# Optimization experiments

Hardware: AMD Instinct MI355X
Metric: run time of the kernel (lower is better)

The kernel has to match this reference:

```python
import jax, jax.numpy as jnp
import numpy as np

E = 1024
H = 16
HD = 64
LN_EPS = 1e-5


def _layernorm(x, g, b):
    mu = jnp.mean(x, axis=-1, keepdims=True)
    var = jnp.mean((x - mu) ** 2, axis=-1, keepdims=True)
    return (x - mu) * jax.lax.rsqrt(var + LN_EPS) * g + b


def _positional(L):
    # PositionalEncoding: stepper = 1/10000^(arange(0,E,2)/E); cat(sin, cos) -> [L, E]
    stepper = 1.0 / (10000.0 ** (jnp.arange(0, E, 2, dtype=jnp.float32) / E))
    args = jnp.arange(L, dtype=jnp.float32)[:, None] * stepper[None, :]  # [L, E/2]
    return jnp.concatenate([jnp.sin(args), jnp.cos(args)], axis=1)  # [L, E]


def setup_inputs() -> dict:
    key = jax.random.key(0)
    ks = jax.random.split(key, 8)
    s = 1.0 / np.sqrt(E)
    return {
        "sequences": jax.random.normal(ks[0], (4, 2048, E), dtype=jnp.float32),
        "W_q": jax.random.normal(ks[1], (E, E), dtype=jnp.float32) * s,
        "W_k": jax.random.normal(ks[2], (E, E), dtype=jnp.float32) * s,
        "W_v": jax.random.normal(ks[3], (E, E), dtype=jnp.float32) * s,
        "W_o": jax.random.normal(ks[4], (E, E), dtype=jnp.float32) * s,
        "ln1_g": jnp.ones((E,), jnp.float32),
        "ln1_b": jnp.zeros((E,), jnp.float32),
        "lin_W": jax.random.normal(ks[5], (E, E), dtype=jnp.float32) * s,  # torch Linear weight [out,in]
        "lin_b": jnp.zeros((E,), jnp.float32),
        "ln2_g": jnp.ones((E,), jnp.float32),
        "ln2_b": jnp.zeros((E,), jnp.float32),
    }


def reference(sequences, W_q, W_k, W_v, W_o, ln1_g, ln1_b, lin_W, lin_b, ln2_g, ln2_b):
    B, L, _ = sequences.shape
    x = sequences + _positional(L)[None]  # add positional embeddings
    # projections (no bias)
    q = (x @ W_q).reshape(B, L, H, HD).transpose(0, 2, 1, 3)  # [B,H,L,hd]
    k = (x @ W_k).reshape(B, L, H, HD).transpose(0, 2, 1, 3)
    v = (x @ W_v).reshape(B, L, H, HD).transpose(0, 2, 1, 3)
    # linear (softmax-free) attention: (Q K^T / sqrt(hd)) V
    scores = jnp.einsum("bhqd,bhkd->bhqk", q, k) / jnp.sqrt(jnp.float32(HD))
    ctx = jnp.einsum("bhqk,bhkd->bhqd", scores, v)
    ctx = ctx.transpose(0, 2, 1, 3).reshape(B, L, E)
    attn_out = ctx @ W_o
    h = _layernorm(x + attn_out, ln1_g, ln1_b)
    ff = jax.nn.relu(h @ lin_W.T + lin_b)
    return _layernorm(ff + h, ln2_g, ln2_b)
```

## Files before the change

kernel.cpp:

```cpp
#include <hip/hip_runtime.h>
#include <cstdint>

typedef unsigned short u16;
typedef __bf16 bf16x8 __attribute__((ext_vector_type(8)));
typedef float f32x4 __attribute__((ext_vector_type(4)));

__device__ __forceinline__ u16 f2bf(float f) {
    unsigned u = __float_as_uint(f);
    u += 0x7fffu + ((u >> 16) & 1u);
    return (u16)(u >> 16);
}
__device__ __forceinline__ float bf2f(u16 h) {
    return __uint_as_float(((unsigned)h) << 16);
}

__device__ __forceinline__ void lds16(const void* g, void* l) {
    __builtin_amdgcn_global_load_lds(
        (const __attribute__((address_space(1))) void*)g,
        (__attribute__((address_space(3))) void*)l, 16, 0, 0);
}

__device__ __forceinline__ float pos_term(int l, int e) {
    const float c = -13.287712379549449f / 512.0f;
    int ii = e & 511;
    float st  = exp2f(c * (float)ii);
    float arg = (float)l * st;
    return (e < 512) ? sinf(arg) : cosf(arg);
}

__global__ __launch_bounds__(256) void prep_all(const float* __restrict__ seq,
                                                const float* __restrict__ wq,
                                                const float* __restrict__ wk,
                                                const float* __restrict__ wv,
                                                const float* __restrict__ wl,
                                                u16* __restrict__ xb,
                                                u16* __restrict__ xt,
                                                u16* __restrict__ wt) {
    const int bx = blockIdx.x;
    const int t = threadIdx.x;
    if (bx < 4096) {
        __shared__ u16 tb[64][33];
        const int rt = bx >> 5, ct = bx & 31;
        const int r0 = rt * 64, c0 = ct * 32;
        const int r_l = t >> 2, c8 = (t & 3) * 8;
        const int row = r0 + r_l, l = row & 2047;
        const float* sp = seq + (size_t)row * 1024 + c0 + c8;
        float4 a0 = ((const float4*)sp)[0];
        float4 a1 = ((const float4*)sp)[1];
        float v[8] = {a0.x, a0.y, a0.z, a0.w, a1.x, a1.y, a1.z, a1.w};
        u16 ob[8];
#pragma unroll
        for (int jj = 0; jj < 8; jj++) {
            v[jj] += pos_term(l, c0 + c8 + jj);
            ob[jj] = f2bf(v[jj]);
            tb[r_l][c8 + jj] = ob[jj];
        }
        u16* xp = xb + (size_t)row * 1024 + c0 + c8;
        ((ushort4*)xp)[0] = *(const ushort4*)&ob[0];
        ((ushort4*)xp)[1] = *(const ushort4*)&ob[4];
        __syncthreads();
        const int c_l = t >> 3, r8 = (t & 7) * 8;
        u16 tv[8];
#pragma unroll
        for (int jj = 0; jj < 8; jj++) tv[jj] = tb[r8 + jj][c_l];
        u16* tp = xt + (size_t)(c0 + c_l) * 8192 + r0 + r8;
        ((ushort4*)tp)[0] = *(const ushort4*)&tv[0];
        ((ushort4*)tp)[1] = *(const ushort4*)&tv[4];
        return;
    }
    const int idx = bx - 4096;
    const int mat = idx >> 10, bxw = idx & 1023;
    const int gx = bxw & 31, gy = bxw >> 5;
    const int tx = t & 31, ty = t >> 5;
    const float* src = (mat == 0) ? wq : (mat == 1) ? wk : (mat == 2) ? wv : wl;
    u16* dst = wt + (size_t)mat * 1024 * 1024;
    if (mat == 0 || mat == 3) {
        int col = gx * 32 + tx, row0 = gy * 32;
#pragma unroll
        for (int j = 0; j < 32; j += 8)
            dst[(size_t)(row0 + ty + j) * 1024 + col] = f2bf(src[(size_t)(row0 + ty + j) * 1024 + col]);
    } else {
        __shared__ float tile[32][33];
        int col = gx * 32 + tx, row0 = gy * 32;
#pragma unroll
        for (int j = 0; j < 32; j += 8)
            tile[ty + j][tx] = src[(size_t)(row0 + ty + j) * 1024 + col];
        __syncthreads();
        int col2 = gy * 32 + tx, row20 = gx * 32;
#pragma unroll
        for (int j = 0; j < 32; j += 8)
            dst[(size_t)(row20 + ty + j) * 1024 + col2] = f2bf(tile[tx][ty + j]);
    }
}

__global__ __launch_bounds__(256) void gram_kernel(const u16* __restrict__ xt,
                                                   u16* __restrict__ G) {
    __shared__ __align__(16) u16 lds[32768];
    const int t = threadIdx.x;
    const int nwg = gridDim.x;
    int bid = (int)blockIdx.x;
    bid = (bid & 7) * (nwg >> 3) + (bid >> 3);
    const int bt = bid >> 6, tile6 = bid & 63;
    const int tm = tile6 >> 3, tn = tile6 & 7;
    const size_t m0 = (size_t)tm << 7, n0 = (size_t)tn << 7;
    const int w = t >> 6, lane = t & 63;
    const int wr = w >> 1, wc = w & 1;
    const size_t lda = 8192;
    const u16* A = xt + (size_t)bt * 2048;

    const int r0 = t >> 3;
    const int ksrc = (t & 7) ^ (r0 & 7);
    const u16* sA = A + (m0 + r0) * lda + ksrc * 8;
    const u16* sB = A + (n0 + r0) * lda + ksrc * 8;
    const size_t st = (size_t)32 * lda;

    const int kx = lane & 7;
    const int ks0 = (((lane >> 4) ^ kx) << 3);
    const int ks1 = (((4 + (lane >> 4)) ^ kx) << 3);
    const int ao = ((wr << 6) | (lane & 15)) << 6;
    const int bo = 8192 + ((((wc << 6) | (lane & 15))) << 6);

    f32x4 acc[4][4];
#pragma unroll
    for (int i = 0; i < 4; i++)
#pragma unroll
        for (int j = 0; j < 4; j++)
#pragma unroll
            for (int r = 0; r < 4; r++) acc[i][j][r] = 0.0f;

#define STAGEG(bb, ko)                                                        \
    do {                                                                      \
        u16* dA_ = lds + (bb) * 16384 + (w << 9);                             \
        u16* dB_ = dA_ + 8192;                                                \
        _Pragma("unroll")                                                     \
        for (int j_ = 0; j_ < 4; j_++) {                                      \
            lds16(sA + (ko) + j_ * st, dA_ + j_ * 2048);                      \
            lds16(sB + (ko) + j_ * st, dB_ + j_ * 2048);                      \
        }                                                                     \
    } while (0)

    const int NT = 32;
    STAGEG(0, 0);
    for (int kt = 0; kt < NT; kt++) {
        const int b = kt & 1;
        asm volatile("" ::: "memory");
        if (kt + 1 < NT) {
            STAGEG(b ^ 1, (size_t)(kt + 1) << 6);
            asm volatile("s_waitcnt vmcnt(8)" ::: "memory");
        } else {
            asm volatile("s_waitcnt vmcnt(0)" ::: "memory");
        }
        __builtin_amdgcn_s_barrier();
        asm volatile("" ::: "memory");
        const u16* Lb = lds + b * 16384;
#pragma unroll
        for (int kc = 0; kc < 2; kc++) {
            const int ksl = kc ? ks1 : ks0;
            bf16x8 af[4], bfr[4];
#pragma unroll
            for (int i = 0; i < 4; i++)
                af[i] = *reinterpret_cast<const bf16x8*>(Lb + ao + i * 1024 + ksl);
#pragma unroll
            for (int j = 0; j < 4; j++)
                bfr[j] = *reinterpret_cast<const bf16x8*>(Lb + bo + j * 1024 + ksl);
            __builtin_amdgcn_s_setprio(1);
#pragma unroll
            for (int i = 0; i < 4; i++)
#pragma unroll
                for (int j = 0; j < 4; j++)
                    acc[i][j] = __builtin_amdgcn_mfma_f32_16x16x32_bf16(af[i], bfr[j], acc[i][j], 0, 0, 0);
            __builtin_amdgcn_s_setprio(0);
        }
        asm volatile("" ::: "memory");
        __builtin_amdgcn_s_barrier();
    }
#undef STAGEG

    u16* C = G + ((size_t)bt << 20);
    const int crow = (lane >> 4) << 2, ccol = lane & 15;
#pragma unroll
    for (int i = 0; i < 4; i++)
#pragma unroll
        for (int j = 0; j < 4; j++) {
            size_t row = m0 + (wr << 6) + (i << 4) + crow;
            size_t col = n0 + (wc << 6) + (j << 4) + ccol;
#pragma unroll
            for (int r = 0; r < 4; r++)
                C[(row + r) * 1024 + col] = f2bf(acc[i][j][r]);
        }
}

template <int EPI>
__global__ __launch_bounds__(512) void gemm8p(const u16* __restrict__ A,
                                              const u16* __restrict__ Bt,
                                              void* __restrict__ Cv,
                                              const float* __restrict__ bias,
                                              int N, int K, int lda, size_t bstride) {
    __shared__ __align__(16) u16 lds[49152];
    const int t = threadIdx.x;
    const int ntn = N >> 8;
    const int nwg = gridDim.x;
    int bid = (int)blockIdx.x;
    bid = (bid & 7) * (nwg >> 3) + (bid >> 3);
    const int tm = bid / ntn, tn = bid - tm * ntn;
    const size_t m0 = (size_t)tm << 7, n0 = (size_t)tn << 8;
    const int w = t >> 6, lane = t & 63;
    const int wr = w >> 2, wc = w & 3;
    const u16* Bt_e = Bt + (bstride ? (m0 >> 11) * bstride : 0);

    const int r0 = t >> 3;
    const int ksrc = (t & 7) ^ (r0 & 7);
    const u16* sA0 = A + (m0 + r0) * (size_t)lda + ksrc * 8;
    const u16* sA1 = sA0 + (size_t)64 * lda;
    const u16* sB0 = Bt_e + (n0 + r0) * (size_t)K + ksrc * 8;
    const u16* sB1 = sB0 + (size_t)64 * K;
    const u16* sB2 = sB0 + (size_t)128 * K;
    const u16* sB3 = sB0 + (size_t)192 * K;
    u16* dstW = lds + (w << 9);

    const int ao = ((wr << 6) | (lane & 15)) << 6;
    const int bo = 8192 + ((((wc << 6) | (lane & 15))) << 6);
    const int kx = lane & 7;
    const int ks0 = (((lane >> 4) ^ kx) << 3);
    const int ks1 = (((4 + (lane >> 4)) ^ kx) << 3);

    f32x4 acc[4][4];
#pragma unroll
    for (int i = 0; i < 4; i++)
#pragma unroll
        for (int j = 0; j < 4; j++)
#pragma unroll
            for (int r = 0; r < 4; r++) acc[i][j][r] = 0.0f;

    const int NT = K >> 6;
    lds16(sA0, dstW);          lds16(sA1, dstW + 4096);
    lds16(sB0, dstW + 8192);   lds16(sB1, dstW + 12288);
    lds16(sB2, dstW + 16384);  lds16(sB3, dstW + 20480);

    for (int kt = 0; kt < NT; kt++) {
        const int b = kt & 1;
        asm volatile("" ::: "memory");
        if (kt + 1 < NT) {
            const size_t ko = (size_t)(kt + 1) << 6;
            u16* d = dstW + (b ^ 1) * 24576;
            lds16(sA0 + ko, d);          lds16(sA1 + ko, d + 4096);
            lds16(sB0 + ko, d + 8192);   lds16(sB1 + ko, d + 12288);
            lds16(sB2 + ko, d + 16384);  lds16(sB3 + ko, d + 20480);
            asm volatile("s_waitcnt vmcnt(6)" ::: "memory");
        } else {
            asm volatile("s_waitcnt vmcnt(0)" ::: "memory");
        }
        __builtin_amdgcn_s_barrier();
        asm volatile("" ::: "memory");
        const u16* Lb = lds + b * 24576;
#pragma unroll
        for (int kc = 0; kc < 2; kc++) {
            const int ksl = kc ? ks1 : ks0;
            bf16x8 af[4], bfr[4];
#pragma unroll
            for (int i = 0; i < 4; i++)
                af[i] = *reinterpret_cast<const bf16x8*>(Lb + ao + i * 1024 + ksl);
#pragma unroll
            for (int j = 0; j < 4; j++)
                bfr[j] = *reinterpret_cast<const bf16x8*>(Lb + bo + j * 1024 + ksl);
            __builtin_amdgcn_s_setprio(1);
#pragma unroll
            for (int i = 0; i < 4; i++)
#pragma unroll
                for (int j = 0; j < 4; j++)
                    acc[i][j] = __builtin_amdgcn_mfma_f32_16x16x32_bf16(af[i], bfr[j], acc[i][j], 0, 0, 0);
            __builtin_amdgcn_s_setprio(0);
        }
        asm volatile("" ::: "memory");
        __builtin_amdgcn_s_barrier();
    }

    const int crow = (lane >> 4) << 2, ccol = lane & 15;
#pragma unroll
    for (int i = 0; i < 4; i++)
#pragma unroll
        for (int j = 0; j < 4; j++) {
            size_t row = m0 + (wr << 6) + (i << 4) + crow;
            size_t col = n0 + (wc << 6) + (j << 4) + ccol;
#pragma unroll
            for (int r = 0; r < 4; r++) {
                float v = acc[i][j][r];
                if (EPI == 3) { v += bias[col]; v = fmaxf(v, 0.0f); }
                ((u16*)Cv)[(row + r) * (size_t)N + col] = f2bf(v);
            }
        }
}

template <bool ADDI>
__global__ __launch_bounds__(256) void gemm128(const u16* __restrict__ A,
                                               const u16* __restrict__ Bt,
                                               u16* __restrict__ C,
                                               int N, int K, int lda) {
    __shared__ __align__(16) u16 lds[32768];
    const int t = threadIdx.x;
    const int ntn = N >> 7;
    const int nwg = gridDim.x;
    int bid = (int)blockIdx.x;
    bid = (bid & 7) * (nwg >> 3) + (bid >> 3);
    const int tm = bid / ntn, tn = bid - tm * ntn;
    const size_t m0 = (size_t)tm << 7, n0 = (size_t)tn << 7;
    const int w = t >> 6, lane = t & 63;
    const int wr = w >> 1, wc = w & 1;

    const int r0 = t >> 3;
    const int ksrc = (t & 7) ^ (r0 & 7);
    const u16* sA = A + (m0 + r0) * (size_t)lda + ksrc * 8;
    const u16* sB = Bt + (n0 + r0) * (size_t)K + ksrc * 8;
    const size_t stA = (size_t)32 * lda, stB = (size_t)32 * K;

    const int kx = lane & 7;
    const int ks0 = (((lane >> 4) ^ kx) << 3);
    const int ks1 = (((4 + (lane >> 4)) ^ kx) << 3);
    const int ao = ((wr << 6) | (lane & 15)) << 6;
    const int bo = 8192 + ((((wc << 6) | (lane & 15))) << 6);

    f32x4 acc[4][4];
#pragma unroll
    for (int i = 0; i < 4; i++)
#pragma unroll
        for (int j = 0; j < 4; j++)
#pragma unroll
            for (int r = 0; r < 4; r++) acc[i][j][r] = 0.0f;

#define STAGE128(bb, ko)                                                      \
    do {                                                                      \
        u16* dA_ = lds + (bb) * 16384 + (w << 9);                             \
        u16* dB_ = dA_ + 8192;                                                \
        _Pragma("unroll")                                                     \
        for (int j_ = 0; j_ < 4; j_++) {                                      \
            lds16(sA + (ko) + j_ * stA, dA_ + j_ * 2048);                     \
            lds16(sB + (ko) + j_ * stB, dB_ + j_ * 2048);                     \
        }                                                                     \
    } while (0)

    const int NT = K >> 6;
    STAGE128(0, 0);
    for (int kt = 0; kt < NT; kt++) {
        const int b = kt & 1;
        asm volatile("" ::: "memory");
        if (kt + 1 < NT) {
            STAGE128(b ^ 1, (size_t)(kt + 1) << 6);
            asm volatile("s_waitcnt vmcnt(8)" ::: "memory");
        } else {
            asm volatile("s_waitcnt vmcnt(0)" ::: "memory");
        }
        __builtin_amdgcn_s_barrier();
        asm volatile("" ::: "memory");
        const u16* Lb = lds + b * 16384;
#pragma unroll
        for (int kc = 0; kc < 2; kc++) {
            const int ksl = kc ? ks1 : ks0;
            bf16x8 af[4], bfr[4];
#pragma unroll
            for (int i = 0; i < 4; i++)
                af[i] = *reinterpret_cast<const bf16x8*>(Lb + ao + i * 1024 + ksl);
#pragma unroll
            for (int j = 0; j < 4; j++)
                bfr[j] = *reinterpret_cast<const bf16x8*>(Lb + bo + j * 1024 + ksl);
            __builtin_amdgcn_s_setprio(1);
#pragma unroll
            for (int i = 0; i < 4; i++)
#pragma unroll
                for (int j = 0; j < 4; j++)
                    acc[i][j] = __builtin_amdgcn_mfma_f32_16x16x32_bf16(af[i], bfr[j], acc[i][j], 0, 0, 0);
            __builtin_amdgcn_s_setprio(0);
        }
        asm volatile("" ::: "memory");
        __builtin_amdgcn_s_barrier();
    }
#undef STAGE128

    const int crow = (lane >> 4) << 2, ccol = lane & 15;
#pragma unroll
    for (int i = 0; i < 4; i++)
#pragma unroll
        for (int j = 0; j < 4; j++) {
            size_t row = m0 + (wr << 6) + (i << 4) + crow;
            size_t col = n0 + (wc << 6) + (j << 4) + ccol;
#pragma unroll
            for (int r = 0; r < 4; r++) {
                float v = acc[i][j][r];
                if (ADDI && col == ((row + r) & 1023)) v += 1.0f;
                C[(row + r) * (size_t)N + col] = f2bf(v);
            }
        }
}

__global__ __launch_bounds__(256) void ktv_small(const u16* __restrict__ T,
                                                 const u16* __restrict__ WkT,
                                                 float* __restrict__ ktv) {
    const int bh = blockIdx.x, ig = blockIdx.y;
    const int b = bh >> 4, h = bh & 15;
    const int t = threadIdx.x;
    const int j = t & 63;
    const int dq = __builtin_amdgcn_readfirstlane(t >> 6);
    const u16* Tb = T + ((size_t)b * 1024) * 1024 + h * 64;
    const u16* Wk = WkT + (size_t)(h * 64 + ig * 16) * 1024;
    float acc[16];
#pragma unroll
    for (int i = 0; i < 16; i++) acc[i] = 0.0f;
    const int d0 = dq * 256;
    for (int d = d0; d < d0 + 256; d += 2) {
        float tv0 = bf2f(Tb[(size_t)d * 1024 + j]);
        float tv1 = bf2f(Tb[(size_t)(d + 1) * 1024 + j]);
#pragma unroll
        for (int i = 0; i < 16; i++) {
            unsigned wv = *(const unsigned*)(Wk + i * 1024 + d);
            acc[i] += bf2f((u16)wv) * tv0 + bf2f((u16)(wv >> 16)) * tv1;
        }
    }
    __shared__ float red[4][16][64];
#pragma unroll
    for (int i = 0; i < 16; i++) red[t >> 6][i][j] = acc[i];
    __syncthreads();
    if (t < 64) {
#pragma unroll
        for (int i = 0; i < 16; i++) {
            float s = red[0][i][j] + red[1][i][j] + red[2][i][j] + red[3][i][j];
            ktv[((size_t)bh << 12) + (ig * 16 + i) * 64 + j] = s;
        }
    }
}

__global__ __launch_bounds__(256) void wprime_kernel(const float* __restrict__ ktv,
                                                     const float* __restrict__ Wo,
                                                     u16* __restrict__ wp) {
    const int n = blockIdx.x * 256 + threadIdx.x;
    const int h = blockIdx.y, b = blockIdx.z;
    const float* kt = ktv + ((size_t)(b * 16 + h) << 12);
    float acc[64];
#pragma unroll
    for (int i = 0; i < 64; i++) acc[i] = 0.0f;
    for (int j = 0; j < 64; j++) {
        float w = Wo[(size_t)(h * 64 + j) * 1024 + n];
#pragma unroll
        for (int i = 0; i < 64; i++) acc[i] += kt[i * 64 + j] * w;
    }
    u16* o = wp + ((size_t)b << 20) + (size_t)n * 1024 + h * 64;
    u16 ob[64];
#pragma unroll
    for (int i = 0; i < 64; i++) ob[i] = f2bf(acc[i] * 0.125f);
#pragma unroll
    for (int i = 0; i < 8; i++)
        ((uint4*)o)[i] = ((const uint4*)ob)[i];
}

__global__ __launch_bounds__(256) void ln1_kernel(const u16* __restrict__ xr,
                                                  const float* __restrict__ g,
                                                  const float* __restrict__ be,
                                                  u16* __restrict__ outB) {
    __shared__ float sm[4];
    const int row = blockIdx.x, t = threadIdx.x;
    const ushort4 xv = ((const ushort4*)(xr + (size_t)row * 1024))[t];
    float x0 = bf2f(xv.x), x1 = bf2f(xv.y), x2 = bf2f(xv.z), x3 = bf2f(xv.w);
    float s = x0 + x1 + x2 + x3;
#pragma unroll
    for (int off = 32; off > 0; off >>= 1) s += __shfl_down(s, off);
    if ((t & 63) == 0) sm[t >> 6] = s;
    __syncthreads();
    const float mean = (sm[0] + sm[1] + sm[2] + sm[3]) * (1.0f / 1024.0f);
    __syncthreads();
    x0 -= mean; x1 -= mean; x2 -= mean; x3 -= mean;
    float s2 = x0 * x0 + x1 * x1 + x2 * x2 + x3 * x3;
#pragma unroll
    for (int off = 32; off > 0; off >>= 1) s2 += __shfl_down(s2, off);
    if ((t & 63) == 0) sm[t >> 6] = s2;
    __syncthreads();
    const float var = (sm[0] + sm[1] + sm[2] + sm[3]) * (1.0f / 1024.0f);
    const float rs = rsqrtf(var + 1e-5f);
    const float4 gv = ((const float4*)g)[t];
    const float4 bv = ((const float4*)be)[t];
    ushort4 ob;
    ob.x = f2bf(x0 * rs * gv.x + bv.x);
    ob.y = f2bf(x1 * rs * gv.y + bv.y);
    ob.z = f2bf(x2 * rs * gv.z + bv.z);
    ob.w = f2bf(x3 * rs * gv.w + bv.w);
    ((ushort4*)(outB + (size_t)row * 1024))[t] = ob;
}

__global__ __launch_bounds__(256) void ln2_kernel(const u16* __restrict__ ff,
                                                  const u16* __restrict__ h1,
                                                  const float* __restrict__ g,
                                                  const float* __restrict__ be,
                                                  float* __restrict__ outF) {
    __shared__ float sm[4];
    const int row = blockIdx.x, t = threadIdx.x;
    const ushort4 fv = ((const ushort4*)(ff + (size_t)row * 1024))[t];
    const ushort4 hv = ((const ushort4*)(h1 + (size_t)row * 1024))[t];
    float x0 = bf2f(fv.x) + bf2f(hv.x), x1 = bf2f(fv.y) + bf2f(hv.y);
    float x2 = bf2f(fv.z) + bf2f(hv.z), x3 = bf2f(fv.w) + bf2f(hv.w);
    float s = x0 + x1 + x2 + x3;
#pragma unroll
    for (int off = 32; off > 0; off >>= 1) s += __shfl_down(s, off);
    if ((t & 63) == 0) sm[t >> 6] = s;
    __syncthreads();
    const float mean = (sm[0] + sm[1] + sm[2] + sm[3]) * (1.0f / 1024.0f);
    __syncthreads();
    x0 -= mean; x1 -= mean; x2 -= mean; x3 -= mean;
    float s2 = x0 * x0 + x1 * x1 + x2 * x2 + x3 * x3;
#pragma unroll
    for (int off = 32; off > 0; off >>= 1) s2 += __shfl_down(s2, off);
    if ((t & 63) == 0) sm[t >> 6] = s2;
    __syncthreads();
    const float var = (sm[0] + sm[1] + sm[2] + sm[3]) * (1.0f / 1024.0f);
    const float rs = rsqrtf(var + 1e-5f);
    const float4 gv = ((const float4*)g)[t];
    const float4 bv = ((const float4*)be)[t];
    float4 o;
    o.x = x0 * rs * gv.x + bv.x;
    o.y = x1 * rs * gv.y + bv.y;
    o.z = x2 * rs * gv.z + bv.z;
    o.w = x3 * rs * gv.w + bv.w;
    ((float4*)(outF + (size_t)row * 1024))[t] = o;
}

extern "C" void kernel_launch(void* const* d_in, const int* in_sizes, int n_in,
                              void* d_out, int out_size, void* d_ws, size_t ws_size,
                              hipStream_t stream) {
    const float* seq = (const float*)d_in[0];
    const float* Wq  = (const float*)d_in[1];
    const float* Wk  = (const float*)d_in[2];
    const float* Wv  = (const float*)d_in[3];
    const float* Wo  = (const float*)d_in[4];
    const float* g1  = (const float*)d_in[5];
    const float* b1  = (const float*)d_in[6];
    const float* Wl  = (const float*)d_in[7];
    const float* bl  = (const float*)d_in[8];
    const float* g2  = (const float*)d_in[9];
    const float* b2  = (const float*)d_in[10];

    char* ws = (char*)d_ws;
    const size_t MB = 1024 * 1024;
    u16*   x_bf    = (u16*)(ws + 0);
    u16*   wt      = (u16*)(ws + 16 * MB);
    u16*   xT      = (u16*)(ws + 24 * MB);
    u16*   G       = (u16*)(ws + 40 * MB);
    u16*   Tm      = (u16*)(ws + 48 * MB);
    float* ktv     = (float*)(ws + 56 * MB);
    u16*   wpr     = (u16*)(ws + 57 * MB);
    u16*   wcomb   = (u16*)(ws + 65 * MB);
    u16*   attnres = (u16*)(ws + 73 * MB);
    u16*   h1b     = (u16*)(ws + 89 * MB);
    u16*   ffb     = (u16*)(ws + 105 * MB);

    prep_all<<<dim3(4096 + 4096), dim3(256), 0, stream>>>(seq, Wq, Wk, Wv, Wl,
                                                          x_bf, xT, wt);
    gram_kernel<<<dim3(256), dim3(256), 0, stream>>>(xT, G);
    gemm128<false><<<dim3(256), dim3(256), 0, stream>>>(G, wt + (size_t)2 * MB, Tm,
                                                        1024, 1024, 1024);
    ktv_small<<<dim3(64, 4), dim3(256), 0, stream>>>(Tm, wt + (size_t)1 * MB, ktv);
    wprime_kernel<<<dim3(4, 16, 4), dim3(256), 0, stream>>>(ktv, Wo, wpr);
    gemm128<true><<<dim3(256), dim3(256), 0, stream>>>(wpr, wt, wcomb, 1024, 1024, 1024);
    gemm8p<2><<<dim3(256), dim3(512), 0, stream>>>(x_bf, wcomb, attnres, nullptr,
                                                   1024, 1024, 1024, (size_t)1024 * 1024);
    ln1_kernel<<<dim3(8192), dim3(256), 0, stream>>>(attnres, g1, b1, h1b);
    gemm8p<3><<<dim3(256), dim3(512), 0, stream>>>(h1b, wt + (size_t)3 * MB, ffb,
                                                   bl, 1024, 1024, 1024, 0);
    ln2_kernel<<<dim3(8192), dim3(256), 0, stream>>>(ffb, h1b, g2, b2, (float*)d_out);
}
```

Baseline: 225.3 us.

## Split K^T V reduction across 16 blocks with shared-memory tiling and reduce kernel

Replaces the ktv_small kernel, which did long strided scalar dot products over 256 grid blocks, with a split-K outer-product kernel over 1024 blocks. Each block stages 8-row tiles of K and V in shared memory and accumulates a 4x4 register tile. A separate reduce kernel then sums the 16 partials. The prep kernel additionally writes an untransposed bf16 copy of W_k to feed the new layout. This costs an extra launch, extra workspace traffic for the partials, and more prep work.

```diff
diff --git a/kernel.cpp b/kernel.cpp
--- a/kernel.cpp
+++ b/kernel.cpp
@@ -72,9 +72,10 @@
     const int mat = idx >> 10, bxw = idx & 1023;
     const int gx = bxw & 31, gy = bxw >> 5;
     const int tx = t & 31, ty = t >> 5;
-    const float* src = (mat == 0) ? wq : (mat == 1) ? wk : (mat == 2) ? wv : wl;
+    const float* src = (mat == 0) ? wq : (mat == 1) ? wk : (mat == 2) ? wv
+                     : (mat == 3) ? wl : wk;
     u16* dst = wt + (size_t)mat * 1024 * 1024;
-    if (mat == 0 || mat == 3) {
+    if (mat == 0 || mat == 3 || mat == 4) {
         int col = gx * 32 + tx, row0 = gy * 32;
 #pragma unroll
         for (int j = 0; j < 32; j += 8)
@@ -391,40 +392,51 @@
         }
 }
 
-__global__ __launch_bounds__(256) void ktv_small(const u16* __restrict__ T,
-                                                 const u16* __restrict__ WkT,
-                                                 float* __restrict__ ktv) {
-    const int bh = blockIdx.x, ig = blockIdx.y;
+__global__ __launch_bounds__(256) void ktv2_kernel(const u16* __restrict__ WkD,
+                                                   const u16* __restrict__ Tm,
+                                                   float* __restrict__ part) {
+    const int bh = blockIdx.x, split = blockIdx.y;
     const int b = bh >> 4, h = bh & 15;
-    const int t = threadIdx.x;
-    const int j = t & 63;
-    const int dq = __builtin_amdgcn_readfirstlane(t >> 6);
-    const u16* Tb = T + ((size_t)b * 1024) * 1024 + h * 64;
-    const u16* Wk = WkT + (size_t)(h * 64 + ig * 16) * 1024;
+    const u16* Kp = WkD + h * 64;
+    const u16* Vp = Tm + (size_t)b * 1024 * 1024 + h * 64;
+    __shared__ float ks[8][64], vs[8][64];
     float acc[16];
 #pragma unroll
     for (int i = 0; i < 16; i++) acc[i] = 0.0f;
-    const int d0 = dq * 256;
-    for (int d = d0; d < d0 + 256; d += 2) {
-        float tv0 = bf2f(Tb[(size_t)d * 1024 + j]);
-        float tv1 = bf2f(Tb[(size_t)(d + 1) * 1024 + j]);
-#pragma unroll
-        for (int i = 0; i < 16; i++) {
-            unsigned wv = *(const unsigned*)(Wk + i * 1024 + d);
-            acc[i] += bf2f((u16)wv) * tv0 + bf2f((u16)(wv >> 16)) * tv1;
-        }
-    }
-    __shared__ float red[4][16][64];
-#pragma unroll
-    for (int i = 0; i < 16; i++) red[t >> 6][i][j] = acc[i];
-    __syncthreads();
-    if (t < 64) {
-#pragma unroll
-        for (int i = 0; i < 16; i++) {
-            float s = red[0][i][j] + red[1][i][j] + red[2][i][j] + red[3][i][j];
-            ktv[((size_t)bh << 12) + (ig * 16 + i) * 64 + j] = s;
-        }
-    }
+    const int t = threadIdx.x, r = t >> 4, c = t & 15;
+    const int lr = t >> 5, lc = (t & 31) * 2;
+    for (int l0 = split * 64; l0 < split * 64 + 64; l0 += 8) {
+        unsigned kk = *(const unsigned*)(Kp + (size_t)(l0 + lr) * 1024 + lc);
+        unsigned vv = *(const unsigned*)(Vp + (size_t)(l0 + lr) * 1024 + lc);
+        ks[lr][lc] = bf2f((u16)kk); ks[lr][lc + 1] = bf2f((u16)(kk >> 16));
+        vs[lr][lc] = bf2f((u16)vv); vs[lr][lc + 1] = bf2f((u16)(vv >> 16));
+        __syncthreads();
+#pragma unroll
+        for (int i = 0; i < 8; i++) {
+            float kvr[4], vw[4];
+#pragma unroll
+            for (int a = 0; a < 4; a++) { kvr[a] = ks[i][r + 16 * a]; vw[a] = vs[i][c + 16 * a]; }
+#pragma unroll
+            for (int a = 0; a < 4; a++)
+#pragma unroll
+                for (int q = 0; q < 4; q++) acc[a * 4 + q] += kvr[a] * vw[q];
+        }
+        __syncthreads();
+    }
+    float* o = part + ((size_t)split * 64 + bh) * 4096;
+#pragma unroll
+    for (int a = 0; a < 4; a++)
+#pragma unroll
+        for (int q = 0; q < 4; q++) o[(r + 16 * a) * 64 + (c + 16 * q)] = acc[a * 4 + q];
+}
+
+__global__ __launch_bounds__(256) void ktv_reduce(const float* __restrict__ part,
+                                                  float* __restrict__ ktv) {
+    int i = blockIdx.x * 256 + threadIdx.x;
+    float s = 0.0f;
+#pragma unroll
+    for (int sp = 0; sp < 16; sp++) s += part[(size_t)sp * 262144 + i];
+    ktv[i] = s;
 }
 
 __global__ __launch_bounds__(256) void wprime_kernel(const float* __restrict__ ktv,
@@ -538,22 +550,24 @@
     const size_t MB = 1024 * 1024;
     u16*   x_bf    = (u16*)(ws + 0);
     u16*   wt      = (u16*)(ws + 16 * MB);
-    u16*   xT      = (u16*)(ws + 24 * MB);
-    u16*   G       = (u16*)(ws + 40 * MB);
-    u16*   Tm      = (u16*)(ws + 48 * MB);
-    float* ktv     = (float*)(ws + 56 * MB);
-    u16*   wpr     = (u16*)(ws + 57 * MB);
-    u16*   wcomb   = (u16*)(ws + 65 * MB);
-    u16*   attnres = (u16*)(ws + 73 * MB);
-    u16*   h1b     = (u16*)(ws + 89 * MB);
-    u16*   ffb     = (u16*)(ws + 105 * MB);
-
-    prep_all<<<dim3(4096 + 4096), dim3(256), 0, stream>>>(seq, Wq, Wk, Wv, Wl,
+    u16*   xT      = (u16*)(ws + 26 * MB);
+    u16*   G       = (u16*)(ws + 42 * MB);
+    u16*   Tm      = (u16*)(ws + 50 * MB);
+    float* kpart   = (float*)(ws + 58 * MB);
+    float* ktv     = (float*)(ws + 74 * MB);
+    u16*   wpr     = (u16*)(ws + 75 * MB);
+    u16*   wcomb   = (u16*)(ws + 83 * MB);
+    u16*   attnres = (u16*)(ws + 91 * MB);
+    u16*   h1b     = (u16*)(ws + 107 * MB);
+    u16*   ffb     = (u16*)(ws + 123 * MB);
+
+    prep_all<<<dim3(4096 + 5120), dim3(256), 0, stream>>>(seq, Wq, Wk, Wv, Wl,
                                                           x_bf, xT, wt);
     gram_kernel<<<dim3(256), dim3(256), 0, stream>>>(xT, G);
     gemm128<false><<<dim3(256), dim3(256), 0, stream>>>(G, wt + (size_t)2 * MB, Tm,
                                                         1024, 1024, 1024);
-    ktv_small<<<dim3(64, 4), dim3(256), 0, stream>>>(Tm, wt + (size_t)1 * MB, ktv);
+    ktv2_kernel<<<dim3(64, 16), dim3(256), 0, stream>>>(wt + (size_t)4 * MB, Tm, kpart);
+    ktv_reduce<<<dim3(1024), dim3(256), 0, stream>>>(kpart, ktv);
     wprime_kernel<<<dim3(4, 16, 4), dim3(256), 0, stream>>>(ktv, Wo, wpr);
     gemm128<true><<<dim3(256), dim3(256), 0, stream>>>(wpr, wt, wcomb, 1024, 1024, 1024);
     gemm8p<2><<<dim3(256), dim3(512), 0, stream>>>(x_bf, wcomb, attnres, nullptr,
```

Result: faster. 186.4 us (-17.2%).
